# Performance work log

Measured on AMD Instinct MI355X. Metric: run time of the kernel, lower is better.

Reference implementation:

```python
import jax, jax.numpy as jnp
import numpy as np

N_JOBS, N_MACH = 30, 20
N = N_JOBS * N_MACH          # 600 nodes
IN_DIM = 2
H = 128                      # hidden_dim_feature_extractor
HA = 256                     # hidden_dim_actor
HC = 256                     # hidden_dim_critic
E = 9600                     # edges
BN_EPS = 1e-5


def setup_inputs() -> dict:
    key = jax.random.key(0)
    ks = jax.random.split(key, 16)
    init = lambda k, shp: (jax.random.normal(k, shp, jnp.float32) * 0.05)
    d = {
        "features": jax.random.normal(ks[0], (N, IN_DIM), jnp.float32),
        "edge_index": jax.random.randint(ks[1], (2, E), 0, N, jnp.int32),
        # GIN layer 0 MLP: Linear(IN,H) -> BN -> ReLU -> Linear(H,H)
        "g0_W0": init(ks[2], (IN_DIM, H)), "g0_b0": jnp.zeros((H,), jnp.float32),
        "g0_gamma": jnp.ones((H,), jnp.float32), "g0_beta": jnp.zeros((H,), jnp.float32),
        "g0_W1": init(ks[3], (H, H)), "g0_b1": jnp.zeros((H,), jnp.float32),
        # GIN layer 1 MLP: Linear(H,H) -> BN -> ReLU -> Linear(H,H)
        "g1_W0": init(ks[4], (H, H)), "g1_b0": jnp.zeros((H,), jnp.float32),
        "g1_gamma": jnp.ones((H,), jnp.float32), "g1_beta": jnp.zeros((H,), jnp.float32),
        "g1_W1": init(ks[5], (H, H)), "g1_b1": jnp.zeros((H,), jnp.float32),
        # actor MLP: Linear(3H,HA) -> ReLU -> Linear(HA,1)
        "a_W0": init(ks[6], (3 * H, HA)), "a_b0": jnp.zeros((HA,), jnp.float32),
        "a_W1": init(ks[7], (HA, 1)), "a_b1": jnp.zeros((1,), jnp.float32),
        # critic MLP: Linear(H,HC) -> ReLU -> Linear(HC,1)
        "c_W0": init(ks[8], (H, HC)), "c_b0": jnp.zeros((HC,), jnp.float32),
        "c_W1": init(ks[9], (HC, 1)), "c_b1": jnp.zeros((1,), jnp.float32),
    }
    return d


def _gin_mlp(h, W0, b0, gamma, beta, W1, b1):
    # Linear -> BatchNorm(train-mode batch stats) -> ReLU -> Linear
    h1 = h @ W0 + b0
    mu = h1.mean(axis=0)
    var = h1.var(axis=0)
    h1 = gamma * (h1 - mu) * jax.lax.rsqrt(var + BN_EPS) + beta
    return jax.nn.relu(h1) @ W1 + b1


def reference(features, edge_index,
              g0_W0, g0_b0, g0_gamma, g0_beta, g0_W1, g0_b1,
              g1_W0, g1_b0, g1_gamma, g1_beta, g1_W1, g1_b1,
              a_W0, a_b0, a_W1, a_b1,
              c_W0, c_b0, c_W1, c_b1):
    src, dst = edge_index[0], edge_index[1]

    def gin(x, *mlp_params):
        # GINConv with eps=0: MLP(x + sum_{j in N(i)} x_j)
        agg = jax.ops.segment_sum(x[src], dst, num_segments=N)
        return _gin_mlp(x + agg, *mlp_params)

    h = gin(features, g0_W0, g0_b0, g0_gamma, g0_beta, g0_W1, g0_b1)
    h = gin(h, g1_W0, g1_b0, g1_gamma, g1_beta, g1_W1, g1_b1)   # (N, H)

    # graph pooling: (ones/N) @ h  == mean over nodes
    ge = h.mean(axis=0, keepdims=True)                           # (1, H)
    value = jax.nn.relu(ge @ c_W0 + c_b0) @ c_W1 + c_b1          # (1, 1)

    # s_a_pairs row k (k = i*N + j): [ge, h[j] (tile), h[i] (repeat_interleave)]
    # Fuse concat + first actor matmul by splitting a_W0 into three H-blocks.
    Ws, Wn1, Wn2 = a_W0[:H], a_W0[H:2 * H], a_W0[2 * H:]
    pre = (ge @ Ws + a_b0)[None, :, :] + (h @ Wn1)[None, :, :] + (h @ Wn2)[:, None, :]
    logits = jax.nn.relu(pre).reshape(N * N, HA) @ a_W1 + a_b1   # (N^2, 1)
    pi = jax.nn.softmax(logits, axis=0)
    return pi, value
```

## Files before the change

kernel.cpp:

```cpp
#include <hip/hip_runtime.h>
#include <math.h>

#define N_NODES 600
#define N_EDGES 9600
#define HDIM    128
#define HA      256
#define HC      256
#define NN      360000
#define BN_EPS  1e-5f
#define NTILE   361

#define OFF_U      0
#define OFF_BCONST 1200
#define OFF_BF     1456
#define OFF_SUMZ   1584
#define OFF_SUMZ2  1712
#define OFF_R1SUM  1840
#define OFF_RACC   1968
#define OFF_SUMA   2736
#define OFF_CSR    3248
#define OFF_WF     13456
#define OFF_WC1    29840
#define OFF_WC2    62608
#define OFF_WGS    95376
#define OFF_Z      128144
#define OFF_A      204944
#define OFF_B      358544

typedef _Float16 h2 __attribute__((ext_vector_type(2)));
typedef _Float16 h4 __attribute__((ext_vector_type(4)));
typedef _Float16 h8 __attribute__((ext_vector_type(8)));

__device__ __forceinline__ float dot2acc(h2 a, h2 b, float c) {
#if __has_builtin(__builtin_amdgcn_fdot2)
  return __builtin_amdgcn_fdot2(a, b, c, false);
#else
  return c + (float)a.x * (float)b.x + (float)a.y * (float)b.y;
#endif
}

__device__ __forceinline__ h2 relu2(h2 x) {
  h2 z = {(_Float16)0, (_Float16)0};
#if __has_builtin(__builtin_elementwise_max)
  return __builtin_elementwise_max(x, z);
#else
  h2 r;
  r.x = x.x > z.x ? x.x : z.x;
  r.y = x.y > z.y ? x.y : z.y;
  return r;
#endif
}

__device__ __forceinline__ h4 toh4(float4 v) {
  h4 r;
  r.x = (_Float16)v.x; r.y = (_Float16)v.y;
  r.z = (_Float16)v.z; r.w = (_Float16)v.w;
  return r;
}

struct KP {
  const float* feat; const int* ei;
  const float *g0W0, *g0ga, *g0be, *g0W1, *g0b1;
  const float *g1W0, *g1ga, *g1be, *g1W1, *g1b1;
  const float *aW0, *ab0, *aW1;
  const float *cW0, *cb0, *cW1, *cb1;
  float* ws; float* out;
};

__global__ __launch_bounds__(256) void k_indep(KP p) {
  __shared__ float sm[1536];
  const int b = blockIdx.x, t = threadIdx.x;

  if (b < 25) {
    float* us = sm;
    if (t < 48) us[t] = 0.f;
    __syncthreads();
    const int lo = b * 24, hi = lo + 24;
    for (int e = t; e < N_EDGES; e += 256) {
      int d = p.ei[N_EDGES + e];
      if (d >= lo && d < hi) {
        int s = p.ei[e];
        atomicAdd(&us[2 * (d - lo)],     p.feat[2 * s]);
        atomicAdd(&us[2 * (d - lo) + 1], p.feat[2 * s + 1]);
      }
    }
    __syncthreads();
    if (t < 48) p.ws[OFF_U + b * 48 + t] = us[t] + p.feat[b * 48 + t];
  } else if (b == 25) {
    int* si = (int*)sm;
    int* cnt = si; int* bs = si + 600; int* off = si + 856;
    int* rs_g = (int*)(p.ws + OFF_CSR);
    int* src_g = rs_g + 604;
    for (int i = t; i < 600; i += 256) cnt[i] = 0;
    __syncthreads();
    for (int e = t; e < N_EDGES; e += 256) atomicAdd(&cnt[p.ei[N_EDGES + e]], 1);
    __syncthreads();
    int lsum = 0;
    if (t < 200) lsum = cnt[3 * t] + cnt[3 * t + 1] + cnt[3 * t + 2];
    bs[t] = lsum; __syncthreads();
    for (int d = 1; d < 256; d <<= 1) {
      int v = (t >= d) ? bs[t - d] : 0;
      __syncthreads();
      bs[t] += v;
      __syncthreads();
    }
    if (t < 200) {
      int base = bs[t] - lsum;
      off[3 * t] = base;
      off[3 * t + 1] = base + cnt[3 * t];
      off[3 * t + 2] = base + cnt[3 * t] + cnt[3 * t + 1];
    }
    if (t == 0) off[600] = N_EDGES;
    __syncthreads();
    for (int i = t; i < 601; i += 256) rs_g[i] = off[i];
    for (int i = t; i < 600; i += 256) cnt[i] = off[i];
    __syncthreads();
    for (int e = t; e < N_EDGES; e += 256) {
      int d = p.ei[N_EDGES + e];
      int pos = atomicAdd(&cnt[d], 1);
      src_g[pos] = p.ei[e];
    }
  } else if (b < 42) {
    int o = (b - 26) * 1024 + t * 4;
    int j = o >> 7, c = o & 127;
    float4 acc = make_float4(0, 0, 0, 0);
#pragma unroll 8
    for (int m = 0; m < HDIM; m++) {
      float w = p.g0W1[j * HDIM + m];
      const float4 v = *(const float4*)(p.g1W0 + m * HDIM + c);
      acc.x += w * v.x; acc.y += w * v.y; acc.z += w * v.z; acc.w += w * v.w;
    }
    *(float4*)(p.ws + OFF_WF + j * HDIM + c) = acc;
  } else {
    p.ws[OFF_RACC + t] = 0.f;
    if (t < 128) {
      float a2 = 0.f;
#pragma unroll 8
      for (int m = 0; m < HDIM; m++) a2 += p.g0b1[m] * p.g1W0[m * HDIM + t];
      p.ws[OFF_BF + t] = a2;
      p.ws[OFF_SUMZ + t] = 0.f;
      p.ws[OFF_SUMZ2 + t] = 0.f;
      p.ws[OFF_R1SUM + t] = 0.f;
    }
  }
}

__global__ __launch_bounds__(256) void k_zagg(KP p) {
  __shared__ float2 u2[600];
  __shared__ float bn[384];
  __shared__ float r0agg[512];
  __shared__ float red[256];
  __shared__ float wred[24];
  const int b = blockIdx.x, t = threadIdx.x;

  if (b >= 150) {
    if (b < 246) {
      int o = (b - 150) * 1024 + t * 4;
      int mat = o >> 15, rem = o & 32767;
      int j = rem >> 8, k = rem & 255;
      int rowbase = (mat == 0) ? HDIM : (mat == 1 ? 2 * HDIM : 0);
      const float* aw = p.aW0 + rowbase * HA + k;
      float4 acc = make_float4(0, 0, 0, 0);
#pragma unroll 8
      for (int m = 0; m < HDIM; m++) {
        float w = p.g1W1[j * HDIM + m];
        const float4 v = *(const float4*)(aw + m * HA);
        acc.x += w * v.x; acc.y += w * v.y; acc.z += w * v.z; acc.w += w * v.w;
      }
      int dst = (mat == 0) ? OFF_WC1 : (mat == 1 ? OFF_WC2 : OFF_WGS);
      *(float4*)(p.ws + dst + j * HA + k) = acc;
    } else {
      float acc = 0.f;
#pragma unroll 8
      for (int m = 0; m < HDIM; m++) {
        float gb = p.g1b1[m];
        acc += gb * (p.aW0[m * HA + t] + p.aW0[(HDIM + m) * HA + t] +
                     p.aW0[(2 * HDIM + m) * HA + t]);
      }
      p.ws[OFF_BCONST + t] = p.ab0[t] + acc;
    }
    return;
  }

  const int n0 = b * 4;
  const float2* ug = (const float2*)(p.ws + OFF_U);
  for (int i = t; i < 600; i += 256) u2[i] = ug[i];
  __syncthreads();
  float s0 = 0, s1 = 0, s00 = 0, s11 = 0, s01 = 0;
  for (int n = t; n < N_NODES; n += 256) {
    float u0 = u2[n].x, u1 = u2[n].y;
    s0 += u0; s1 += u1; s00 += u0 * u0; s11 += u1 * u1; s01 += u0 * u1;
  }
#pragma unroll
  for (int off = 32; off > 0; off >>= 1) {
    s0  += __shfl_xor(s0, off);  s1  += __shfl_xor(s1, off);
    s00 += __shfl_xor(s00, off); s11 += __shfl_xor(s11, off);
    s01 += __shfl_xor(s01, off);
  }
  const int wv = t >> 6, ln = t & 63;
  if (ln == 0) {
    wred[wv * 5 + 0] = s0;  wred[wv * 5 + 1] = s1;  wred[wv * 5 + 2] = s00;
    wred[wv * 5 + 3] = s11; wred[wv * 5 + 4] = s01;
  }
  __syncthreads();
  if (t < HDIM) {
    float tot[5];
#pragma unroll
    for (int q = 0; q < 5; q++)
      tot[q] = wred[q] + wred[5 + q] + wred[10 + q] + wred[15 + q];
    float m0 = tot[0] / 600.f, m1 = tot[1] / 600.f;
    float v00 = tot[2] / 600.f - m0 * m0;
    float v11 = tot[3] / 600.f - m1 * m1;
    float v01 = tot[4] / 600.f - m0 * m1;
    float W00 = p.g0W0[t], W01 = p.g0W0[HDIM + t];
    float var = W00 * W00 * v00 + W01 * W01 * v11 + 2.f * W00 * W01 * v01;
    float sc = p.g0ga[t] * rsqrtf(var + BN_EPS);
    float mu = m0 * W00 + m1 * W01;
    bn[t] = sc * W00; bn[128 + t] = sc * W01; bn[256 + t] = p.g0be[t] - mu * sc;
  }
  __syncthreads();
  const int* rs = (const int*)(p.ws + OFF_CSR);
  const int* srcv = rs + 604;
#pragma unroll
  for (int pq = 0; pq < 2; pq++) {
    int idx = pq * 256 + t, n = idx >> 7, c = idx & 127, node = n0 + n;
    float b0c = bn[c], b1c = bn[128 + c], b2c = bn[256 + c];
    float2 uo = u2[node];
    float acc = fmaxf(uo.x * b0c + uo.y * b1c + b2c, 0.f);
    int e0 = rs[node], e1 = rs[node + 1];
    for (int e = e0; e < e1; e++) {
      float2 us = u2[srcv[e]];
      acc += fmaxf(us.x * b0c + us.y * b1c + b2c, 0.f);
    }
    r0agg[n * 128 + c] = acc;
  }
  __syncthreads();
  const float* Wf = p.ws + OFF_WF;
  const float* bf = p.ws + OFF_BF;
  float zs = 0.f, zs2 = 0.f;
#pragma unroll
  for (int pq = 0; pq < 2; pq++) {
    int idx = pq * 256 + t, n = idx >> 7, c = idx & 127, node = n0 + n;
    const float* row = r0agg + n * 128;
    int deg = rs[node + 1] - rs[node];
    float acc = (1.f + (float)deg) * bf[c];
#pragma unroll 8
    for (int j = 0; j < HDIM; j++) acc += row[j] * Wf[j * HDIM + c];
    p.ws[OFF_Z + node * HDIM + c] = acc;
    zs += acc; zs2 += acc * acc;
  }
  red[t] = zs; __syncthreads();
  if (t < 128) atomicAdd(&p.ws[OFF_SUMZ + t], red[t] + red[t + 128]);
  __syncthreads();
  red[t] = zs2; __syncthreads();
  if (t < 128) atomicAdd(&p.ws[OFF_SUMZ2 + t], red[t] + red[t + 128]);
}

__global__ __launch_bounds__(256) void k_rab(KP p) {
  __shared__ float r1[4 * 128];
  __shared__ float scl[128], shf[128], rsum4[128];
  const int b = blockIdx.x, t = threadIdx.x, n0 = b * 4;
  if (t < 128) {
    float mu = p.ws[OFF_SUMZ + t] * (1.f / 600.f);
    float var = p.ws[OFF_SUMZ2 + t] * (1.f / 600.f) - mu * mu;
    float sc = p.g1ga[t] * rsqrtf(var + BN_EPS);
    scl[t] = sc; shf[t] = p.g1be[t] - mu * sc;
  }
  __syncthreads();
#pragma unroll
  for (int pq = 0; pq < 2; pq++) {
    int idx = pq * 256 + t, n = idx >> 7, j = idx & 127;
    float z = p.ws[OFF_Z + (n0 + n) * HDIM + j];
    r1[n * 128 + j] = fmaxf(z * scl[j] + shf[j], 0.f);
  }
  __syncthreads();
  if (t < 128) {
    float s = r1[t] + r1[128 + t] + r1[256 + t] + r1[384 + t];
    rsum4[t] = s;
    atomicAdd(&p.ws[OFF_R1SUM + t], s);
  }
  __syncthreads();
  const float* wc1 = p.ws + OFF_WC1;
  const float* wc2 = p.ws + OFF_WC2;
  const float* wgs = p.ws + OFF_WGS;
  float a0 = 0, a1 = 0, a2 = 0, a3 = 0, b0 = 0, b1 = 0, b2 = 0, b3 = 0, rc = 0;
#pragma unroll 4
  for (int j = 0; j < HDIM; j++) {
    float w1 = wc1[j * HA + t], w2 = wc2[j * HA + t], wg = wgs[j * HA + t];
    float r0v = r1[j], r1v = r1[128 + j], r2v = r1[256 + j], r3v = r1[384 + j];
    a0 += r0v * w1; a1 += r1v * w1; a2 += r2v * w1; a3 += r3v * w1;
    b0 += r0v * w2; b1 += r1v * w2; b2 += r2v * w2; b3 += r3v * w2;
    rc += rsum4[j] * wg;
  }
  atomicAdd(&p.ws[OFF_RACC + t], rc);
  float* A = p.ws + OFF_A; float* Bm = p.ws + OFF_B;
  A[n0 * HA + t] = a0; A[(n0 + 1) * HA + t] = a1;
  A[(n0 + 2) * HA + t] = a2; A[(n0 + 3) * HA + t] = a3;
  Bm[n0 * HA + t] = b0; Bm[(n0 + 1) * HA + t] = b1;
  Bm[(n0 + 2) * HA + t] = b2; Bm[(n0 + 3) * HA + t] = b3;
}

__global__ __launch_bounds__(256) void k_heads(KP p) {
  __shared__ h4 AsL[2048];
  __shared__ h4 BsL[2048];
  __shared__ h4 wlp[64];
  __shared__ h4 hsp[64];
  __shared__ float hsl[256];
  __shared__ float ge[128];
  __shared__ float geh[128];
  __shared__ float red[256];
  const int b = blockIdx.x, t = threadIdx.x;

  hsl[t] = p.ws[OFF_RACC + t] * (1.f / 600.f) + p.ws[OFF_BCONST + t];

  if (b == 0) {
    if (t < 128) ge[t] = p.ws[OFF_R1SUM + t] * (1.f / 600.f);
    __syncthreads();
    if (t < 128) {
      float a0 = p.g1b1[t], a1 = 0.f, a2 = 0.f, a3 = 0.f;
#pragma unroll 4
      for (int j = 0; j < HDIM; j += 4) {
        a0 += ge[j]     * p.g1W1[(j)     * HDIM + t];
        a1 += ge[j + 1] * p.g1W1[(j + 1) * HDIM + t];
        a2 += ge[j + 2] * p.g1W1[(j + 2) * HDIM + t];
        a3 += ge[j + 3] * p.g1W1[(j + 3) * HDIM + t];
      }
      geh[t] = (a0 + a1) + (a2 + a3);
    }
    __syncthreads();
    {
      float v0 = p.cb0[t], v1 = 0.f, v2 = 0.f, v3 = 0.f;
#pragma unroll 4
      for (int c = 0; c < HDIM; c += 4) {
        v0 += geh[c]     * p.cW0[(c)     * HC + t];
        v1 += geh[c + 1] * p.cW0[(c + 1) * HC + t];
        v2 += geh[c + 2] * p.cW0[(c + 2) * HC + t];
        v3 += geh[c + 3] * p.cW0[(c + 3) * HC + t];
      }
      float v = fmaxf((v0 + v1) + (v2 + v3), 0.f);
      red[t] = v * p.cW1[t];
    }
    __syncthreads();
    for (int off = 128; off > 0; off >>= 1) {
      if (t < off) red[t] += red[t + off];
      __syncthreads();
    }
    if (t == 0) p.out[NN] = red[0] + p.cb1[0];
  }
  __syncthreads();
  if (t < 64) {
    wlp[t] = toh4(*(const float4*)(p.aW1 + 4 * t));
    hsp[t] = toh4(*(const float4*)(hsl + 4 * t));
  }
  __syncthreads();

  const int tj = b % 19, ti = b / 19;
  const int j0 = tj * 32, i0 = ti * 32;
  const float* A  = p.ws + OFF_A;
  const float* Bm = p.ws + OFF_B;
#pragma unroll
  for (int q = 0; q < 8; q++) {
    int f = q * 256 + t;
    int r = f >> 6;
    int c4 = f & 63;
    int k = c4 * 4;
    int sw = c4 * 32 + (r ^ (c4 & 30));
    float4 av = (j0 + r < N_NODES) ? *(const float4*)(A + (j0 + r) * HA + k)
                                   : make_float4(0, 0, 0, 0);
    AsL[sw] = toh4(av) + hsp[c4];
    float4 bv = (i0 + r < N_NODES) ? *(const float4*)(Bm + (i0 + r) * HA + k)
                                   : make_float4(0, 0, 0, 0);
    BsL[sw] = toh4(bv);
  }
  __syncthreads();

  const int tx = t & 15, ty = t >> 4;
  const int jl = tx * 2, il = ty * 2;
  float a00 = 0, a01 = 0, a10 = 0, a11 = 0;
#pragma unroll 8
  for (int kk2 = 0; kk2 < 64; kk2++) {
    int s = kk2 & 30;
    h8 va = *(h8*)&AsL[kk2 * 32 + (jl ^ s)];
    h8 vb = *(h8*)&BsL[kk2 * 32 + (il ^ s)];
    h4 vw = wlp[kk2];
    h2 wlo = __builtin_shufflevector(vw, vw, 0, 1);
    h2 whi = __builtin_shufflevector(vw, vw, 2, 3);
    h2 aj0lo = __builtin_shufflevector(va, va, 0, 1);
    h2 aj0hi = __builtin_shufflevector(va, va, 2, 3);
    h2 aj1lo = __builtin_shufflevector(va, va, 4, 5);
    h2 aj1hi = __builtin_shufflevector(va, va, 6, 7);
    h2 bi0lo = __builtin_shufflevector(vb, vb, 0, 1);
    h2 bi0hi = __builtin_shufflevector(vb, vb, 2, 3);
    h2 bi1lo = __builtin_shufflevector(vb, vb, 4, 5);
    h2 bi1hi = __builtin_shufflevector(vb, vb, 6, 7);
    a00 = dot2acc(relu2(aj0lo + bi0lo), wlo, a00);
    a00 = dot2acc(relu2(aj0hi + bi0hi), whi, a00);
    a01 = dot2acc(relu2(aj1lo + bi0lo), wlo, a01);
    a01 = dot2acc(relu2(aj1hi + bi0hi), whi, a01);
    a10 = dot2acc(relu2(aj0lo + bi1lo), wlo, a10);
    a10 = dot2acc(relu2(aj0hi + bi1hi), whi, a10);
    a11 = dot2acc(relu2(aj1lo + bi1lo), wlo, a11);
    a11 = dot2acc(relu2(aj1hi + bi1hi), whi, a11);
  }

  const int gi = i0 + il, gj = j0 + jl;
  const bool vi0 = gi < N_NODES, vi1 = gi + 1 < N_NODES;
  const bool vj0 = gj < N_NODES, vj1 = gj + 1 < N_NODES;
  float s = 0.f;
  if (vi0 && vj0) { float e = __expf(a00); p.out[gi * N_NODES + gj] = e; s += e; }
  if (vi0 && vj1) { float e = __expf(a01); p.out[gi * N_NODES + gj + 1] = e; s += e; }
  if (vi1 && vj0) { float e = __expf(a10); p.out[(gi + 1) * N_NODES + gj] = e; s += e; }
  if (vi1 && vj1) { float e = __expf(a11); p.out[(gi + 1) * N_NODES + gj + 1] = e; s += e; }
  __syncthreads();
  red[t] = s;
  __syncthreads();
  for (int off = 128; off > 0; off >>= 1) {
    if (t < off) red[t] += red[t + off];
    __syncthreads();
  }
  if (t == 0) p.ws[OFF_SUMA + b] = red[0];
}

__global__ __launch_bounds__(256) void k_fin(KP p) {
  __shared__ float red[256];
  const int b = blockIdx.x, t = threadIdx.x;
  const float* suma = p.ws + OFF_SUMA;
  float s = (t < NTILE ? suma[t] : 0.f) + (t + 256 < NTILE ? suma[t + 256] : 0.f);
  red[t] = s;
  __syncthreads();
  for (int off = 128; off > 0; off >>= 1) {
    if (t < off) red[t] += red[t + off];
    __syncthreads();
  }
  const float inv = 1.0f / red[0];
#pragma unroll
  for (int pass = 0; pass < 3; pass++) {
    int f4 = pass * 256 + t;
    if (f4 < 600) {
      int r = f4 / 150, c4 = (f4 % 150) * 4;
      float* pp = p.out + (b * 4 + r) * N_NODES + c4;
      float4 v = *(const float4*)pp;
      v.x *= inv; v.y *= inv; v.z *= inv; v.w *= inv;
      *(float4*)pp = v;
    }
  }
}

extern "C" void kernel_launch(void* const* d_in, const int* in_sizes, int n_in,
                              void* d_out, int out_size, void* d_ws, size_t ws_size,
                              hipStream_t stream) {
  KP p;
  p.feat = (const float*)d_in[0];
  p.ei   = (const int*)  d_in[1];
  p.g0W0 = (const float*)d_in[2];
  p.g0ga = (const float*)d_in[4];  p.g0be = (const float*)d_in[5];
  p.g0W1 = (const float*)d_in[6];  p.g0b1 = (const float*)d_in[7];
  p.g1W0 = (const float*)d_in[8];
  p.g1ga = (const float*)d_in[10]; p.g1be = (const float*)d_in[11];
  p.g1W1 = (const float*)d_in[12]; p.g1b1 = (const float*)d_in[13];
  p.aW0  = (const float*)d_in[14]; p.ab0  = (const float*)d_in[15];
  p.aW1  = (const float*)d_in[16];
  p.cW0  = (const float*)d_in[18]; p.cb0  = (const float*)d_in[19];
  p.cW1  = (const float*)d_in[20]; p.cb1  = (const float*)d_in[21];
  p.ws   = (float*)d_ws;
  p.out  = (float*)d_out;

  k_indep<<<43,    256, 0, stream>>>(p);
  k_zagg <<<247,   256, 0, stream>>>(p);
  k_rab  <<<150,   256, 0, stream>>>(p);
  k_heads<<<NTILE, 256, 0, stream>>>(p);
  k_fin  <<<150,   256, 0, stream>>>(p);
}
```

Measured before the change: 78.41 us.

## Enlarge pairwise actor tile to 48x32 and hoist layer-0 BN stats into prologue

The pairwise actor-head kernel now gives each thread a 3x2 output block (48x32 tile per workgroup) instead of 2x2 (32x32), cutting the grid from 361 to 247 blocks and reusing each loaded A fragment across more rows. The layer-0 batchnorm statistics, previously recomputed redundantly in each of 150 aggregation blocks, are computed once by a new prologue block and stored to workspace. The swizzle mask changes to fit the new LDS layout, and the final-sum kernel is simplified to match. The larger tile adds register and LDS pressure, and the dedicated stats block redoes the full edge scatter serially in one workgroup.

```diff
diff --git a/kernel.cpp b/kernel.cpp
--- a/kernel.cpp
+++ b/kernel.cpp
@@ -8,24 +8,25 @@
 #define HC      256
 #define NN      360000
 #define BN_EPS  1e-5f
-#define NTILE   361
+#define NTILE   247
 
 #define OFF_U      0
-#define OFF_BCONST 1200
-#define OFF_BF     1456
-#define OFF_SUMZ   1584
-#define OFF_SUMZ2  1712
-#define OFF_R1SUM  1840
-#define OFF_RACC   1968
-#define OFF_SUMA   2736
-#define OFF_CSR    3248
-#define OFF_WF     13456
-#define OFF_WC1    29840
-#define OFF_WC2    62608
-#define OFF_WGS    95376
-#define OFF_Z      128144
-#define OFF_A      204944
-#define OFF_B      358544
+#define OFF_BN0    1200
+#define OFF_BCONST 1584
+#define OFF_BF     1840
+#define OFF_SUMZ   1968
+#define OFF_SUMZ2  2096
+#define OFF_R1SUM  2224
+#define OFF_RACC   2352
+#define OFF_SUMA   2608
+#define OFF_CSR    2864
+#define OFF_WF     13072
+#define OFF_WC1    29456
+#define OFF_WC2    62224
+#define OFF_WGS    94992
+#define OFF_Z      127760
+#define OFF_A      204560
+#define OFF_B      358160
 
 typedef _Float16 h2 __attribute__((ext_vector_type(2)));
 typedef _Float16 h4 __attribute__((ext_vector_type(4)));
@@ -88,15 +89,15 @@
     if (t < 48) p.ws[OFF_U + b * 48 + t] = us[t] + p.feat[b * 48 + t];
   } else if (b == 25) {
     int* si = (int*)sm;
-    int* cnt = si; int* bs = si + 600; int* off = si + 856;
+    int* cn = si; int* bs = si + 600; int* off = si + 856;
     int* rs_g = (int*)(p.ws + OFF_CSR);
     int* src_g = rs_g + 604;
-    for (int i = t; i < 600; i += 256) cnt[i] = 0;
-    __syncthreads();
-    for (int e = t; e < N_EDGES; e += 256) atomicAdd(&cnt[p.ei[N_EDGES + e]], 1);
+    for (int i = t; i < 600; i += 256) cn[i] = 0;
+    __syncthreads();
+    for (int e = t; e < N_EDGES; e += 256) atomicAdd(&cn[p.ei[N_EDGES + e]], 1);
     __syncthreads();
     int lsum = 0;
-    if (t < 200) lsum = cnt[3 * t] + cnt[3 * t + 1] + cnt[3 * t + 2];
+    if (t < 200) lsum = cn[3 * t] + cn[3 * t + 1] + cn[3 * t + 2];
     bs[t] = lsum; __syncthreads();
     for (int d = 1; d < 256; d <<= 1) {
       int v = (t >= d) ? bs[t - d] : 0;
@@ -107,21 +108,67 @@
     if (t < 200) {
       int base = bs[t] - lsum;
       off[3 * t] = base;
-      off[3 * t + 1] = base + cnt[3 * t];
-      off[3 * t + 2] = base + cnt[3 * t] + cnt[3 * t + 1];
+      off[3 * t + 1] = base + cn[3 * t];
+      off[3 * t + 2] = base + cn[3 * t] + cn[3 * t + 1];
     }
     if (t == 0) off[600] = N_EDGES;
     __syncthreads();
     for (int i = t; i < 601; i += 256) rs_g[i] = off[i];
-    for (int i = t; i < 600; i += 256) cnt[i] = off[i];
+    for (int i = t; i < 600; i += 256) cn[i] = off[i];
     __syncthreads();
     for (int e = t; e < N_EDGES; e += 256) {
       int d = p.ei[N_EDGES + e];
-      int pos = atomicAdd(&cnt[d], 1);
+      int pos = atomicAdd(&cn[d], 1);
       src_g[pos] = p.ei[e];
     }
-  } else if (b < 42) {
-    int o = (b - 26) * 1024 + t * 4;
+  } else if (b == 26) {
+    float* ua = sm;
+    float* wred = sm + 1200;
+    for (int i = t; i < 1200; i += 256) ua[i] = 0.f;
+    __syncthreads();
+    for (int e = t; e < N_EDGES; e += 256) {
+      int s = p.ei[e], d = p.ei[N_EDGES + e];
+      atomicAdd(&ua[2 * d],     p.feat[2 * s]);
+      atomicAdd(&ua[2 * d + 1], p.feat[2 * s + 1]);
+    }
+    __syncthreads();
+    float s0 = 0, s1 = 0, s00 = 0, s11 = 0, s01 = 0;
+    for (int n = t; n < N_NODES; n += 256) {
+      float u0 = p.feat[2 * n] + ua[2 * n];
+      float u1 = p.feat[2 * n + 1] + ua[2 * n + 1];
+      s0 += u0; s1 += u1; s00 += u0 * u0; s11 += u1 * u1; s01 += u0 * u1;
+    }
+#pragma unroll
+    for (int off = 32; off > 0; off >>= 1) {
+      s0  += __shfl_xor(s0, off);  s1  += __shfl_xor(s1, off);
+      s00 += __shfl_xor(s00, off); s11 += __shfl_xor(s11, off);
+      s01 += __shfl_xor(s01, off);
+    }
+    const int wv = t >> 6, ln = t & 63;
+    if (ln == 0) {
+      wred[wv * 5 + 0] = s0;  wred[wv * 5 + 1] = s1;  wred[wv * 5 + 2] = s00;
+      wred[wv * 5 + 3] = s11; wred[wv * 5 + 4] = s01;
+    }
+    __syncthreads();
+    if (t < HDIM) {
+      float tot[5];
+#pragma unroll
+      for (int q = 0; q < 5; q++)
+        tot[q] = wred[q] + wred[5 + q] + wred[10 + q] + wred[15 + q];
+      float m0 = tot[0] / 600.f, m1 = tot[1] / 600.f;
+      float v00 = tot[2] / 600.f - m0 * m0;
+      float v11 = tot[3] / 600.f - m1 * m1;
+      float v01 = tot[4] / 600.f - m0 * m1;
+      float W00 = p.g0W0[t], W01 = p.g0W0[HDIM + t];
+      float var = W00 * W00 * v00 + W01 * W01 * v11 + 2.f * W00 * W01 * v01;
+      float sc = p.g0ga[t] * rsqrtf(var + BN_EPS);
+      float mu = m0 * W00 + m1 * W01;
+      p.ws[OFF_BN0 + t] = sc * W00;
+      p.ws[OFF_BN0 + 128 + t] = sc * W01;
+      p.ws[OFF_BN0 + 256 + t] = p.g0be[t] - mu * sc;
+    }
+  } else if (b < 43) {
+    int o = (b - 27) * 1024 + t * 4;
     int j = o >> 7, c = o & 127;
     float4 acc = make_float4(0, 0, 0, 0);
 #pragma unroll 8
@@ -150,7 +197,6 @@
   __shared__ float bn[384];
   __shared__ float r0agg[512];
   __shared__ float red[256];
-  __shared__ float wred[24];
   const int b = blockIdx.x, t = threadIdx.x;
 
   if (b >= 150) {
@@ -185,39 +231,7 @@
   const int n0 = b * 4;
   const float2* ug = (const float2*)(p.ws + OFF_U);
   for (int i = t; i < 600; i += 256) u2[i] = ug[i];
-  __syncthreads();
-  float s0 = 0, s1 = 0, s00 = 0, s11 = 0, s01 = 0;
-  for (int n = t; n < N_NODES; n += 256) {
-    float u0 = u2[n].x, u1 = u2[n].y;
-    s0 += u0; s1 += u1; s00 += u0 * u0; s11 += u1 * u1; s01 += u0 * u1;
-  }
-#pragma unroll
-  for (int off = 32; off > 0; off >>= 1) {
-    s0  += __shfl_xor(s0, off);  s1  += __shfl_xor(s1, off);
-    s00 += __shfl_xor(s00, off); s11 += __shfl_xor(s11, off);
-    s01 += __shfl_xor(s01, off);
-  }
-  const int wv = t >> 6, ln = t & 63;
-  if (ln == 0) {
-    wred[wv * 5 + 0] = s0;  wred[wv * 5 + 1] = s1;  wred[wv * 5 + 2] = s00;
-    wred[wv * 5 + 3] = s11; wred[wv * 5 + 4] = s01;
-  }
-  __syncthreads();
-  if (t < HDIM) {
-    float tot[5];
-#pragma unroll
-    for (int q = 0; q < 5; q++)
-      tot[q] = wred[q] + wred[5 + q] + wred[10 + q] + wred[15 + q];
-    float m0 = tot[0] / 600.f, m1 = tot[1] / 600.f;
-    float v00 = tot[2] / 600.f - m0 * m0;
-    float v11 = tot[3] / 600.f - m1 * m1;
-    float v01 = tot[4] / 600.f - m0 * m1;
-    float W00 = p.g0W0[t], W01 = p.g0W0[HDIM + t];
-    float var = W00 * W00 * v00 + W01 * W01 * v11 + 2.f * W00 * W01 * v01;
-    float sc = p.g0ga[t] * rsqrtf(var + BN_EPS);
-    float mu = m0 * W00 + m1 * W01;
-    bn[t] = sc * W00; bn[128 + t] = sc * W01; bn[256 + t] = p.g0be[t] - mu * sc;
-  }
+  for (int i = t; i < 384; i += 256) bn[i] = p.ws[OFF_BN0 + i];
   __syncthreads();
   const int* rs = (const int*)(p.ws + OFF_CSR);
   const int* srcv = rs + 604;
@@ -302,7 +316,7 @@
 
 __global__ __launch_bounds__(256) void k_heads(KP p) {
   __shared__ h4 AsL[2048];
-  __shared__ h4 BsL[2048];
+  __shared__ h4 BsL[3072];
   __shared__ h4 wlp[64];
   __shared__ h4 hsp[64];
   __shared__ float hsl[256];
@@ -354,34 +368,38 @@
   }
   __syncthreads();
 
-  const int tj = b % 19, ti = b / 19;
-  const int j0 = tj * 32, i0 = ti * 32;
+  const int ti = b / 19, tj = b % 19;
+  const int i0 = ti * 48, j0 = tj * 32;
   const float* A  = p.ws + OFF_A;
   const float* Bm = p.ws + OFF_B;
 #pragma unroll
   for (int q = 0; q < 8; q++) {
     int f = q * 256 + t;
-    int r = f >> 6;
-    int c4 = f & 63;
-    int k = c4 * 4;
-    int sw = c4 * 32 + (r ^ (c4 & 30));
+    int r = f >> 6, c4 = f & 63, k = c4 * 4;
     float4 av = (j0 + r < N_NODES) ? *(const float4*)(A + (j0 + r) * HA + k)
                                    : make_float4(0, 0, 0, 0);
-    AsL[sw] = toh4(av) + hsp[c4];
+    AsL[c4 * 32 + (r ^ (c4 & 14))] = toh4(av) + hsp[c4];
+  }
+#pragma unroll
+  for (int q = 0; q < 12; q++) {
+    int f = q * 256 + t;
+    int r = f >> 6, c4 = f & 63, k = c4 * 4;
     float4 bv = (i0 + r < N_NODES) ? *(const float4*)(Bm + (i0 + r) * HA + k)
                                    : make_float4(0, 0, 0, 0);
-    BsL[sw] = toh4(bv);
+    BsL[c4 * 48 + (r ^ (c4 & 14))] = toh4(bv);
   }
   __syncthreads();
 
   const int tx = t & 15, ty = t >> 4;
-  const int jl = tx * 2, il = ty * 2;
-  float a00 = 0, a01 = 0, a10 = 0, a11 = 0;
+  const int jl = tx * 2, il = ty * 3;
+  float a00 = 0, a01 = 0, a10 = 0, a11 = 0, a20 = 0, a21 = 0;
 #pragma unroll 8
   for (int kk2 = 0; kk2 < 64; kk2++) {
-    int s = kk2 & 30;
+    int s = kk2 & 14;
     h8 va = *(h8*)&AsL[kk2 * 32 + (jl ^ s)];
-    h8 vb = *(h8*)&BsL[kk2 * 32 + (il ^ s)];
+    h4 vb0 = BsL[kk2 * 48 + ((il)     ^ s)];
+    h4 vb1 = BsL[kk2 * 48 + ((il + 1) ^ s)];
+    h4 vb2 = BsL[kk2 * 48 + ((il + 2) ^ s)];
     h4 vw = wlp[kk2];
     h2 wlo = __builtin_shufflevector(vw, vw, 0, 1);
     h2 whi = __builtin_shufflevector(vw, vw, 2, 3);
@@ -389,28 +407,40 @@
     h2 aj0hi = __builtin_shufflevector(va, va, 2, 3);
     h2 aj1lo = __builtin_shufflevector(va, va, 4, 5);
     h2 aj1hi = __builtin_shufflevector(va, va, 6, 7);
-    h2 bi0lo = __builtin_shufflevector(vb, vb, 0, 1);
-    h2 bi0hi = __builtin_shufflevector(vb, vb, 2, 3);
-    h2 bi1lo = __builtin_shufflevector(vb, vb, 4, 5);
-    h2 bi1hi = __builtin_shufflevector(vb, vb, 6, 7);
-    a00 = dot2acc(relu2(aj0lo + bi0lo), wlo, a00);
-    a00 = dot2acc(relu2(aj0hi + bi0hi), whi, a00);
-    a01 = dot2acc(relu2(aj1lo + bi0lo), wlo, a01);
-    a01 = dot2acc(relu2(aj1hi + bi0hi), whi, a01);
-    a10 = dot2acc(relu2(aj0lo + bi1lo), wlo, a10);
-    a10 = dot2acc(relu2(aj0hi + bi1hi), whi, a10);
-    a11 = dot2acc(relu2(aj1lo + bi1lo), wlo, a11);
-    a11 = dot2acc(relu2(aj1hi + bi1hi), whi, a11);
+    h2 b0lo = __builtin_shufflevector(vb0, vb0, 0, 1);
+    h2 b0hi = __builtin_shufflevector(vb0, vb0, 2, 3);
+    h2 b1lo = __builtin_shufflevector(vb1, vb1, 0, 1);
+    h2 b1hi = __builtin_shufflevector(vb1, vb1, 2, 3);
+    h2 b2lo = __builtin_shufflevector(vb2, vb2, 0, 1);
+    h2 b2hi = __builtin_shufflevector(vb2, vb2, 2, 3);
+    a00 = dot2acc(relu2(aj0lo + b0lo), wlo, a00);
+    a00 = dot2acc(relu2(aj0hi + b0hi), whi, a00);
+    a01 = dot2acc(relu2(aj1lo + b0lo), wlo, a01);
+    a01 = dot2acc(relu2(aj1hi + b0hi), whi, a01);
+    a10 = dot2acc(relu2(aj0lo + b1lo), wlo, a10);
+    a10 = dot2acc(relu2(aj0hi + b1hi), whi, a10);
+    a11 = dot2acc(relu2(aj1lo + b1lo), wlo, a11);
+    a11 = dot2acc(relu2(aj1hi + b1hi), whi, a11);
+    a20 = dot2acc(relu2(aj0lo + b2lo), wlo, a20);
+    a20 = dot2acc(relu2(aj0hi + b2hi), whi, a20);
+    a21 = dot2acc(relu2(aj1lo + b2lo), wlo, a21);
+    a21 = dot2acc(relu2(aj1hi + b2hi), whi, a21);
   }
 
   const int gi = i0 + il, gj = j0 + jl;
-  const bool vi0 = gi < N_NODES, vi1 = gi + 1 < N_NODES;
+  const bool vi0 = gi < N_NODES, vi1 = gi + 1 < N_NODES, vi2 = gi + 2 < N_NODES;
   const bool vj0 = gj < N_NODES, vj1 = gj + 1 < N_NODES;
   float s = 0.f;
-  if (vi0 && vj0) { float e = __expf(a00); p.out[gi * N_NODES + gj] = e; s += e; }
-  if (vi0 && vj1) { float e = __expf(a01); p.out[gi * N_NODES + gj + 1] = e; s += e; }
-  if (vi1 && vj0) { float e = __expf(a10); p.out[(gi + 1) * N_NODES + gj] = e; s += e; }
-  if (vi1 && vj1) { float e = __expf(a11); p.out[(gi + 1) * N_NODES + gj + 1] = e; s += e; }
+  if (vj0) {
+    if (vi0) { float e = __expf(a00); p.out[(gi)     * N_NODES + gj] = e; s += e; }
+    if (vi1) { float e = __expf(a10); p.out[(gi + 1) * N_NODES + gj] = e; s += e; }
+    if (vi2) { float e = __expf(a20); p.out[(gi + 2) * N_NODES + gj] = e; s += e; }
+  }
+  if (vj1) {
+    if (vi0) { float e = __expf(a01); p.out[(gi)     * N_NODES + gj + 1] = e; s += e; }
+    if (vi1) { float e = __expf(a11); p.out[(gi + 1) * N_NODES + gj + 1] = e; s += e; }
+    if (vi2) { float e = __expf(a21); p.out[(gi + 2) * N_NODES + gj + 1] = e; s += e; }
+  }
   __syncthreads();
   red[t] = s;
   __syncthreads();
@@ -425,8 +455,7 @@
   __shared__ float red[256];
   const int b = blockIdx.x, t = threadIdx.x;
   const float* suma = p.ws + OFF_SUMA;
-  float s = (t < NTILE ? suma[t] : 0.f) + (t + 256 < NTILE ? suma[t + 256] : 0.f);
-  red[t] = s;
+  red[t] = (t < NTILE) ? suma[t] : 0.f;
   __syncthreads();
   for (int off = 128; off > 0; off >>= 1) {
     if (t < off) red[t] += red[t + off];
@@ -465,7 +494,7 @@
   p.ws   = (float*)d_ws;
   p.out  = (float*)d_out;
 
-  k_indep<<<43,    256, 0, stream>>>(p);
+  k_indep<<<44,    256, 0, stream>>>(p);
   k_zagg <<<247,   256, 0, stream>>>(p);
   k_rab  <<<150,   256, 0, stream>>>(p);
   k_heads<<<NTILE, 256, 0, stream>>>(p);
```

New measurement: 86.55 us. 1.1x slower.
